# Performance work log

Measured on AMD Instinct MI355X. Metric: run time of the kernel, lower is better.

The kernel has to match this reference:

```python
import jax, jax.numpy as jnp
import numpy as np
import math

N = 20000      # nodes
E = 640000     # edges (avg degree 32)
G = 128        # g_dim (input features)
H1 = 128       # rgcn output dim
H2 = 128       # transformer output dim
R = 8          # num_relations


def setup_inputs() -> dict:
    key = jax.random.key(0)
    ks = jax.random.split(key, 12)
    x = jax.random.normal(ks[0], (N, G), dtype=jnp.float32)
    edge_index = jax.random.randint(ks[1], (2, E), 0, N)
    edge_type = jax.random.randint(ks[2], (E,), 0, R)
    s_in = 1.0 / math.sqrt(G)
    s_h1 = 1.0 / math.sqrt(H1)
    return {
        'x': x,
        'edge_index': edge_index,
        'edge_type': edge_type,
        # RGCNConv params (per-relation weights + root weight + bias)
        'rgcn_weight': jax.random.normal(ks[3], (R, G, H1), dtype=jnp.float32) * s_in,
        'rgcn_root': jax.random.normal(ks[4], (G, H1), dtype=jnp.float32) * s_in,
        'rgcn_bias': jnp.zeros((H1,), dtype=jnp.float32),
        # TransformerConv params (heads=1): query/key/value + skip linear
        'Wq': jax.random.normal(ks[5], (H1, H2), dtype=jnp.float32) * s_h1,
        'bq': jnp.zeros((H2,), dtype=jnp.float32),
        'Wk': jax.random.normal(ks[6], (H1, H2), dtype=jnp.float32) * s_h1,
        'bk': jnp.zeros((H2,), dtype=jnp.float32),
        'Wv': jax.random.normal(ks[7], (H1, H2), dtype=jnp.float32) * s_h1,
        'bv': jnp.zeros((H2,), dtype=jnp.float32),
        'Ws': jax.random.normal(ks[8], (H1, H2), dtype=jnp.float32) * s_h1,
        'bs': jnp.zeros((H2,), dtype=jnp.float32),
    }


def reference(x, edge_index, edge_type, rgcn_weight, rgcn_root, rgcn_bias,
              Wq, bq, Wk, bk, Wv, bv, Ws, bs):
    n = x.shape[0]
    src, dst = edge_index[0], edge_index[1]

    # ---- RGCNConv (aggr='mean' per relation, root weight + bias) ----
    # transform nodes by every relation, then gather per-edge message
    xr = jnp.einsum('ni,rio->nro', x, rgcn_weight)          # [N, R, H1]
    msg = xr[src, edge_type]                                # [E, H1]
    # per (dst, relation) edge counts for mean aggregation
    cnt = jnp.zeros((n, rgcn_weight.shape[0]), x.dtype).at[dst, edge_type].add(1.0)
    denom = jnp.maximum(cnt[dst, edge_type], 1.0)[:, None]  # [E, 1]
    agg = jnp.zeros((n, rgcn_weight.shape[2]), x.dtype).at[dst].add(msg / denom)
    h = agg + x @ rgcn_root + rgcn_bias
    h = jax.nn.relu(h)

    # ---- TransformerConv (heads=1, concat, root_weight=True) ----
    d = Wq.shape[1]
    q = h @ Wq + bq                                          # [N, H2]
    k = h @ Wk + bk
    v = h @ Wv + bv
    score = jnp.sum(q[dst] * k[src], axis=-1) / math.sqrt(d) # [E]
    # softmax over incoming edges of each destination node
    smax = jax.ops.segment_max(score, dst, num_segments=n)   # [N]
    e = jnp.exp(score - smax[dst])                           # [E]
    den = jax.ops.segment_sum(e, dst, num_segments=n)        # [N]
    alpha = e / jnp.maximum(den[dst], 1e-16)                 # [E]
    out = jax.ops.segment_sum(alpha[:, None] * v[src], dst, num_segments=n)
    out = out + h @ Ws + bs                                  # skip connection
    return jax.nn.relu(out)
```

## Files before the change

### kernel.cpp

```cpp
#include <hip/hip_runtime.h>

typedef unsigned short u16;
typedef unsigned int u32;
typedef __attribute__((ext_vector_type(8))) short short8;
typedef __attribute__((ext_vector_type(4))) float f32x4;

#define NN 20000
#define EE 640000
#define SCAN_BLOCKS 80

__device__ inline u16 f2bf(float f) {
    u32 x = __float_as_uint(f);
    return (u16)((x + 0x7FFFu + ((x >> 16) & 1u)) >> 16);
}
__device__ inline float lo16(u32 w) { return __uint_as_float(w << 16); }
__device__ inline float hi16(u32 w) { return __uint_as_float(w & 0xFFFF0000u); }
__device__ inline u32 packbf(float a, float b) { return ((u32)f2bf(b) << 16) | (u32)f2bf(a); }

#define CT_N (EE / 8)
#define CX_N (NN * 32)
#define WP_N (128 * 1152 + 4 * 128 * 128 + 512)
__global__ __launch_bounds__(256) void prep_count(const int* __restrict__ ei,
                                                  const int* __restrict__ et,
                                                  int* __restrict__ cnt, int* __restrict__ rank,
                                                  const float* __restrict__ x,
                                                  const float* rw, const float* root,
                                                  const float* Wq, const float* Wk,
                                                  const float* Wv, const float* Ws,
                                                  const float* bq, const float* bk,
                                                  const float* bv, const float* bs,
                                                  u16* __restrict__ xb,
                                                  u16* wt1, u16* wt2, float* bcat) {
    int idx = blockIdx.x * 256 + threadIdx.x;
    if (idx < CT_N) {
#pragma unroll
        for (int j = 0; j < 8; j++) {
            int e = idx + j * CT_N;
            int dst = ei[EE + e];
            int r = et[e];
            rank[e] = atomicAdd(&cnt[dst * 8 + r], 1);
        }
        return;
    }
    idx -= CT_N;
    if (idx < CX_N) {
        float4 v = *(const float4*)(x + (size_t)idx * 4);
        uint2 o;
        o.x = packbf(v.x, v.y);
        o.y = packbf(v.z, v.w);
        *(uint2*)(xb + (size_t)idx * 4) = o;
        return;
    }
    idx -= CX_N;
    const int S1 = 128 * 1152, S2 = 4 * 128 * 128;
    if (idx < S1) {
        int o = idx / 1152, k = idx - o * 1152;
        float v = (k < 1024) ? rw[k * 128 + o] : root[(k - 1024) * 128 + o];
        wt1[idx] = f2bf(v);
    } else if (idx < S1 + S2) {
        int j = idx - S1;
        int y = j >> 14, rem = j & 16383, o = rem >> 7, i = rem & 127;
        const float* W = (y == 0) ? Wq : (y == 1) ? Wk : (y == 2) ? Wv : Ws;
        wt2[j] = f2bf(W[i * 128 + o]);
    } else if (idx < S1 + S2 + 512) {
        int j = idx - (S1 + S2);
        int y = j >> 7, c = j & 127;
        const float* b = (y == 0) ? bq : (y == 1) ? bk : (y == 2) ? bv : bs;
        bcat[j] = b[c];
    }
}

__global__ __launch_bounds__(256) void scan_phase1(const int* __restrict__ cnt,
                                                   int* __restrict__ deg_pref,
                                                   int* __restrict__ blk_sums) {
    __shared__ int lds[256];
    int t = threadIdx.x;
    int n = blockIdx.x * 256 + t;
    int d = 0;
    if (n < NN) {
        int4 c0 = *(const int4*)(cnt + n * 8);
        int4 c1 = *(const int4*)(cnt + n * 8 + 4);
        d = c0.x + c0.y + c0.z + c0.w + c1.x + c1.y + c1.z + c1.w;
    }
    lds[t] = d;
    __syncthreads();
    for (int o = 1; o < 256; o <<= 1) {
        int v = (t >= o) ? lds[t - o] : 0;
        __syncthreads();
        lds[t] += v;
        __syncthreads();
    }
    if (n < NN) deg_pref[n] = lds[t];
    if (t == 255) blk_sums[blockIdx.x] = lds[255];
}

__global__ __launch_bounds__(256) void scan_phase3(const int* __restrict__ cnt,
                                                   const int* __restrict__ deg_pref,
                                                   const int* __restrict__ blk_sums,
                                                   int* __restrict__ row_off,
                                                   int* __restrict__ srt) {
    __shared__ int bs_lds[128];
    int t = threadIdx.x;
    if (t < 128) {
        int v = (t < SCAN_BLOCKS) ? blk_sums[t] : 0;
        bs_lds[t] = v;
    }
    __syncthreads();
    if (t < 128) {
        for (int o = 1; o < 128; o <<= 1) {
            int a = (t >= o) ? bs_lds[t - o] : 0;
            __syncthreads();
            bs_lds[t] += a;
            __syncthreads();
        }
    } else {
        for (int o = 1; o < 128; o <<= 1) {
            __syncthreads();
            __syncthreads();
        }
    }
    int blk_excl = (blockIdx.x > 0) ? bs_lds[blockIdx.x - 1] : 0;
    int n = blockIdx.x * 256 + t;
    if (n >= NN) return;
    int4 c0 = *(const int4*)(cnt + n * 8);
    int4 c1 = *(const int4*)(cnt + n * 8 + 4);
    int deg = c0.x + c0.y + c0.z + c0.w + c1.x + c1.y + c1.z + c1.w;
    int start = blk_excl + deg_pref[n] - deg;
    row_off[n] = start;
    int sub = start;
    int o[8];
    o[0] = sub; sub += c0.x;
    o[1] = sub; sub += c0.y;
    o[2] = sub; sub += c0.z;
    o[3] = sub; sub += c0.w;
    o[4] = sub; sub += c1.x;
    o[5] = sub; sub += c1.y;
    o[6] = sub; sub += c1.z;
    o[7] = sub; sub += c1.w;
    *(int4*)(srt + n * 8) = make_int4(o[0], o[1], o[2], o[3]);
    *(int4*)(srt + n * 8 + 4) = make_int4(o[4], o[5], o[6], o[7]);
    if (n == NN - 1) row_off[NN] = sub;
}

__global__ void scatter_kernel(const int* __restrict__ ei, const int* __restrict__ et,
                               const int* __restrict__ srt, const int* __restrict__ rank,
                               int* __restrict__ es) {
    int base = blockIdx.x * 2048 + threadIdx.x;
#pragma unroll
    for (int j = 0; j < 8; j++) {
        int e = base + j * 256;
        if (e < EE) {
            int dst = ei[EE + e];
            int src = ei[e];
            int r = et[e];
            es[srt[dst * 8 + r] + rank[e]] = src;
        }
    }
}

__global__ __launch_bounds__(256) void gemm_rgcn_fused(const u16* __restrict__ xb,
                                                       const int* __restrict__ srt,
                                                       const int* __restrict__ cnt,
                                                       const int* __restrict__ es,
                                                       const u16* __restrict__ Bt1,
                                                       const float* __restrict__ bias1,
                                                       const u16* __restrict__ Wt2,
                                                       const float* __restrict__ bcat,
                                                       u16* __restrict__ Cq, u16* __restrict__ Ckv,
                                                       u16* __restrict__ Cs) {
    __shared__ u16 As[32 * 136];
    __shared__ u16 Bs[128 * 136];
    int tid = threadIdx.x;
    int w = tid >> 6;
    int lane = tid & 63;
    int quad = lane >> 4;
    int ml = lane & 15;
    int mt = w & 1;
    int nq = w >> 1;
    int block_m = blockIdx.x * 32;

    int rbase = tid >> 4;
    int cb = (tid & 15) * 8;

    int node_l = tid >> 3;
    int th = tid & 7;
    int db = th * 16;
    int gnode = block_m + node_l;

    f32x4 acc[4];
#pragma unroll
    for (int i = 0; i < 4; i++) acc[i] = (f32x4){0.f, 0.f, 0.f, 0.f};

#pragma unroll 1
    for (int slot = 0; slot < 9; slot++) {
        int kb = slot * 128;
#pragma unroll
        for (int rep = 0; rep < 8; rep++) {
            int r = rbase + rep * 16;
            short8 val = *(const short8*)(Bt1 + (long)r * 1152 + kb + cb);
            *(short8*)(Bs + r * 136 + cb) = val;
        }
        if (slot < 8) {
            int c = cnt[gnode * 8 + slot];
            int p0 = srt[gnode * 8 + slot];
            float a0 = 0.f, a1 = 0.f, a2 = 0.f, a3 = 0.f, a4 = 0.f, a5 = 0.f, a6 = 0.f, a7 = 0.f;
            float a8 = 0.f, a9 = 0.f, a10 = 0.f, a11 = 0.f, a12 = 0.f, a13 = 0.f, a14 = 0.f, a15 = 0.f;
            int i = 0;
            for (; i + 2 <= c; i += 2) {
                int s0 = es[p0 + i], s1 = es[p0 + i + 1];
                uint4 wa0 = *(const uint4*)(xb + (long)s0 * 128 + db);
                uint4 wa1 = *(const uint4*)(xb + (long)s0 * 128 + db + 8);
                uint4 wb0 = *(const uint4*)(xb + (long)s1 * 128 + db);
                uint4 wb1 = *(const uint4*)(xb + (long)s1 * 128 + db + 8);
                a0 += lo16(wa0.x) + lo16(wb0.x);
                a1 += hi16(wa0.x) + hi16(wb0.x);
                a2 += lo16(wa0.y) + lo16(wb0.y);
                a3 += hi16(wa0.y) + hi16(wb0.y);
                a4 += lo16(wa0.z) + lo16(wb0.z);
                a5 += hi16(wa0.z) + hi16(wb0.z);
                a6 += lo16(wa0.w) + lo16(wb0.w);
                a7 += hi16(wa0.w) + hi16(wb0.w);
                a8 += lo16(wa1.x) + lo16(wb1.x);
                a9 += hi16(wa1.x) + hi16(wb1.x);
                a10 += lo16(wa1.y) + lo16(wb1.y);
                a11 += hi16(wa1.y) + hi16(wb1.y);
                a12 += lo16(wa1.z) + lo16(wb1.z);
                a13 += hi16(wa1.z) + hi16(wb1.z);
                a14 += lo16(wa1.w) + lo16(wb1.w);
                a15 += hi16(wa1.w) + hi16(wb1.w);
            }
            if (i < c) {
                int s0 = es[p0 + i];
                uint4 wa0 = *(const uint4*)(xb + (long)s0 * 128 + db);
                uint4 wa1 = *(const uint4*)(xb + (long)s0 * 128 + db + 8);
                a0 += lo16(wa0.x); a1 += hi16(wa0.x); a2 += lo16(wa0.y); a3 += hi16(wa0.y);
                a4 += lo16(wa0.z); a5 += hi16(wa0.z); a6 += lo16(wa0.w); a7 += hi16(wa0.w);
                a8 += lo16(wa1.x); a9 += hi16(wa1.x); a10 += lo16(wa1.y); a11 += hi16(wa1.y);
                a12 += lo16(wa1.z); a13 += hi16(wa1.z); a14 += lo16(wa1.w); a15 += hi16(wa1.w);
            }
            float inv = 1.0f / (float)(c > 1 ? c : 1);
            uint4 o0 = make_uint4(packbf(a0 * inv, a1 * inv), packbf(a2 * inv, a3 * inv),
                                  packbf(a4 * inv, a5 * inv), packbf(a6 * inv, a7 * inv));
            uint4 o1 = make_uint4(packbf(a8 * inv, a9 * inv), packbf(a10 * inv, a11 * inv),
                                  packbf(a12 * inv, a13 * inv), packbf(a14 * inv, a15 * inv));
            *(uint4*)(As + node_l * 136 + db) = o0;
            *(uint4*)(As + node_l * 136 + db + 8) = o1;
        } else {
#pragma unroll
            for (int rep = 0; rep < 2; rep++) {
                int r = rbase + rep * 16;
                short8 val = *(const short8*)(xb + (long)(block_m + r) * 128 + cb);
                *(short8*)(As + r * 136 + cb) = val;
            }
        }
        __syncthreads();
#pragma unroll
        for (int ks = 0; ks < 4; ks++) {
            short8 af = *(const short8*)(As + (mt * 16 + ml) * 136 + ks * 32 + quad * 8);
#pragma unroll
            for (int nt = 0; nt < 4; nt++) {
                short8 bfr = *(const short8*)(Bs + (nq * 64 + nt * 16 + ml) * 136 + ks * 32 + quad * 8);
                acc[nt] = __builtin_amdgcn_mfma_f32_16x16x32_bf16(af, bfr, acc[nt], 0, 0, 0);
            }
        }
        __syncthreads();
    }
#pragma unroll
    for (int nt = 0; nt < 4; nt++) {
        int col = nq * 64 + nt * 16 + ml;
        float bv = bias1[col];
#pragma unroll
        for (int i = 0; i < 4; i++) {
            int r = mt * 16 + quad * 4 + i;
            As[r * 136 + col] = f2bf(fmaxf(acc[nt][i] + bv, 0.f));
        }
    }
    __syncthreads();

#pragma unroll 1
    for (int y = 0; y < 4; y++) {
#pragma unroll
        for (int rep = 0; rep < 8; rep++) {
            int r = rbase + rep * 16;
            short8 val = *(const short8*)(Wt2 + (long)y * 16384 + (long)r * 128 + cb);
            *(short8*)(Bs + r * 136 + cb) = val;
        }
        __syncthreads();
        f32x4 acc2[4];
#pragma unroll
        for (int i = 0; i < 4; i++) acc2[i] = (f32x4){0.f, 0.f, 0.f, 0.f};
#pragma unroll
        for (int ks = 0; ks < 4; ks++) {
            short8 af = *(const short8*)(As + (mt * 16 + ml) * 136 + ks * 32 + quad * 8);
#pragma unroll
            for (int nt = 0; nt < 4; nt++) {
                short8 bfr = *(const short8*)(Bs + (nq * 64 + nt * 16 + ml) * 136 + ks * 32 + quad * 8);
                acc2[nt] = __builtin_amdgcn_mfma_f32_16x16x32_bf16(af, bfr, acc2[nt], 0, 0, 0);
            }
        }
        u16* C;
        int ldc;
        if (y == 0) { C = Cq; ldc = 128; }
        else if (y == 1) { C = Ckv; ldc = 256; }
        else if (y == 2) { C = Ckv + 128; ldc = 256; }
        else { C = Cs; ldc = 128; }
#pragma unroll
        for (int nt = 0; nt < 4; nt++) {
            int col = nq * 64 + nt * 16 + ml;
            float bv = bcat[y * 128 + col];
#pragma unroll
            for (int i = 0; i < 4; i++) {
                int gr = block_m + mt * 16 + quad * 4 + i;
                C[(long)gr * ldc + col] = f2bf(acc2[nt][i] + bv);
            }
        }
        __syncthreads();
    }
}

__global__ __launch_bounds__(128) void attn_kernel(const u16* __restrict__ q,
                                                   const u16* __restrict__ kv,
                                                   const u16* __restrict__ skip,
                                                   const int* __restrict__ row_off,
                                                   const int* __restrict__ es,
                                                   float* __restrict__ out) {
    int node = blockIdx.x * 8 + (threadIdx.x >> 4);
    int lane = threadIdx.x & 15;
    if (node >= NN) return;
    int p0 = row_off[node], p1 = row_off[node + 1];
    uint4 qw = *(const uint4*)(q + (long)node * 128 + lane * 8);
    float q0 = lo16(qw.x), q1 = hi16(qw.x), q2 = lo16(qw.y), q3 = hi16(qw.y);
    float q4 = lo16(qw.z), q5 = hi16(qw.z), q6 = lo16(qw.w), q7 = hi16(qw.w);
    const float SC = 0.08838834764831845f;
    float l = 0.f;
    float a0 = 0.f, a1 = 0.f, a2 = 0.f, a3 = 0.f, a4 = 0.f, a5 = 0.f, a6 = 0.f, a7 = 0.f;
    int p = p0;
    for (; p + 4 <= p1; p += 4) {
        const u16* b0 = kv + (long)es[p] * 256 + lane * 8;
        const u16* b1 = kv + (long)es[p + 1] * 256 + lane * 8;
        const u16* b2 = kv + (long)es[p + 2] * 256 + lane * 8;
        const u16* b3 = kv + (long)es[p + 3] * 256 + lane * 8;
        uint4 k0 = *(const uint4*)b0;
        uint4 k1 = *(const uint4*)b1;
        uint4 k2 = *(const uint4*)b2;
        uint4 k3 = *(const uint4*)b3;
        uint4 v0 = *(const uint4*)(b0 + 128);
        uint4 v1 = *(const uint4*)(b1 + 128);
        uint4 v2 = *(const uint4*)(b2 + 128);
        uint4 v3 = *(const uint4*)(b3 + 128);
        float t0 = q0 * lo16(k0.x) + q1 * hi16(k0.x) + q2 * lo16(k0.y) + q3 * hi16(k0.y) +
                   q4 * lo16(k0.z) + q5 * hi16(k0.z) + q6 * lo16(k0.w) + q7 * hi16(k0.w);
        float t1 = q0 * lo16(k1.x) + q1 * hi16(k1.x) + q2 * lo16(k1.y) + q3 * hi16(k1.y) +
                   q4 * lo16(k1.z) + q5 * hi16(k1.z) + q6 * lo16(k1.w) + q7 * hi16(k1.w);
        float t2 = q0 * lo16(k2.x) + q1 * hi16(k2.x) + q2 * lo16(k2.y) + q3 * hi16(k2.y) +
                   q4 * lo16(k2.z) + q5 * hi16(k2.z) + q6 * lo16(k2.w) + q7 * hi16(k2.w);
        float t3 = q0 * lo16(k3.x) + q1 * hi16(k3.x) + q2 * lo16(k3.y) + q3 * hi16(k3.y) +
                   q4 * lo16(k3.z) + q5 * hi16(k3.z) + q6 * lo16(k3.w) + q7 * hi16(k3.w);
#pragma unroll
        for (int off = 8; off >= 1; off >>= 1) {
            t0 += __shfl_xor(t0, off, 16);
            t1 += __shfl_xor(t1, off, 16);
            t2 += __shfl_xor(t2, off, 16);
            t3 += __shfl_xor(t3, off, 16);
        }
        float w0 = __expf(fminf(t0 * SC, 70.f));
        float w1 = __expf(fminf(t1 * SC, 70.f));
        float w2 = __expf(fminf(t2 * SC, 70.f));
        float w3 = __expf(fminf(t3 * SC, 70.f));
        l += (w0 + w1) + (w2 + w3);
        a0 += w0 * lo16(v0.x) + w1 * lo16(v1.x) + w2 * lo16(v2.x) + w3 * lo16(v3.x);
        a1 += w0 * hi16(v0.x) + w1 * hi16(v1.x) + w2 * hi16(v2.x) + w3 * hi16(v3.x);
        a2 += w0 * lo16(v0.y) + w1 * lo16(v1.y) + w2 * lo16(v2.y) + w3 * lo16(v3.y);
        a3 += w0 * hi16(v0.y) + w1 * hi16(v1.y) + w2 * hi16(v2.y) + w3 * hi16(v3.y);
        a4 += w0 * lo16(v0.z) + w1 * lo16(v1.z) + w2 * lo16(v2.z) + w3 * lo16(v3.z);
        a5 += w0 * hi16(v0.z) + w1 * hi16(v1.z) + w2 * hi16(v2.z) + w3 * hi16(v3.z);
        a6 += w0 * lo16(v0.w) + w1 * lo16(v1.w) + w2 * lo16(v2.w) + w3 * lo16(v3.w);
        a7 += w0 * hi16(v0.w) + w1 * hi16(v1.w) + w2 * hi16(v2.w) + w3 * hi16(v3.w);
    }
    for (; p < p1; p++) {
        const u16* b = kv + (long)es[p] * 256 + lane * 8;
        uint4 kw = *(const uint4*)b;
        uint4 vw = *(const uint4*)(b + 128);
        float t = q0 * lo16(kw.x) + q1 * hi16(kw.x) + q2 * lo16(kw.y) + q3 * hi16(kw.y) +
                  q4 * lo16(kw.z) + q5 * hi16(kw.z) + q6 * lo16(kw.w) + q7 * hi16(kw.w);
#pragma unroll
        for (int off = 8; off >= 1; off >>= 1) t += __shfl_xor(t, off, 16);
        float w = __expf(fminf(t * SC, 70.f));
        l += w;
        a0 += w * lo16(vw.x);
        a1 += w * hi16(vw.x);
        a2 += w * lo16(vw.y);
        a3 += w * hi16(vw.y);
        a4 += w * lo16(vw.z);
        a5 += w * hi16(vw.z);
        a6 += w * lo16(vw.w);
        a7 += w * hi16(vw.w);
    }
    float invl = (l > 0.f) ? 1.0f / l : 0.f;
    uint4 sw = *(const uint4*)(skip + (long)node * 128 + lane * 8);
    float4 oa, ob;
    oa.x = fmaxf(a0 * invl + lo16(sw.x), 0.f);
    oa.y = fmaxf(a1 * invl + hi16(sw.x), 0.f);
    oa.z = fmaxf(a2 * invl + lo16(sw.y), 0.f);
    oa.w = fmaxf(a3 * invl + hi16(sw.y), 0.f);
    ob.x = fmaxf(a4 * invl + lo16(sw.z), 0.f);
    ob.y = fmaxf(a5 * invl + hi16(sw.z), 0.f);
    ob.z = fmaxf(a6 * invl + lo16(sw.w), 0.f);
    ob.w = fmaxf(a7 * invl + hi16(sw.w), 0.f);
    *(float4*)(out + (long)node * 128 + lane * 8) = oa;
    *(float4*)(out + (long)node * 128 + lane * 8 + 4) = ob;
}

extern "C" void kernel_launch(void* const* d_in, const int* in_sizes, int n_in,
                              void* d_out, int out_size, void* d_ws, size_t ws_size,
                              hipStream_t stream) {
    const float* x = (const float*)d_in[0];
    const int* ei = (const int*)d_in[1];
    const int* et = (const int*)d_in[2];
    const float* rw = (const float*)d_in[3];
    const float* root = (const float*)d_in[4];
    const float* rbias = (const float*)d_in[5];
    const float* Wq = (const float*)d_in[6];
    const float* bq = (const float*)d_in[7];
    const float* Wk = (const float*)d_in[8];
    const float* bk = (const float*)d_in[9];
    const float* Wv = (const float*)d_in[10];
    const float* bv = (const float*)d_in[11];
    const float* Ws = (const float*)d_in[12];
    const float* bs = (const float*)d_in[13];

    char* ws = (char*)d_ws;
    size_t off = 0;
    auto alloc = [&](size_t b) {
        size_t o = off;
        off = (off + b + 255) & ~(size_t)255;
        return o;
    };
    u16* qv = (u16*)(ws + alloc((size_t)NN * 128 * 2));
    u16* kv = (u16*)(ws + alloc((size_t)NN * 256 * 2));
    u16* skip = (u16*)(ws + alloc((size_t)NN * 128 * 2));
    u16* xb = (u16*)(ws + alloc((size_t)NN * 128 * 2));
    u16* wt1 = (u16*)(ws + alloc((size_t)128 * 1152 * 2));
    u16* wt2 = (u16*)(ws + alloc((size_t)4 * 128 * 128 * 2));
    float* bcat = (float*)(ws + alloc((size_t)512 * 4));
    int* cnt = (int*)(ws + alloc((size_t)NN * 8 * 4));
    int* row_off = (int*)(ws + alloc((size_t)(NN + 1) * 4));
    int* srt = (int*)(ws + alloc((size_t)NN * 8 * 4));
    int* deg_pref = (int*)(ws + alloc((size_t)NN * 4));
    int* blk_sums = (int*)(ws + alloc((size_t)128 * 4));
    int* rank = (int*)(ws + alloc((size_t)EE * 4));
    int* es = (int*)(ws + alloc((size_t)EE * 4));
    (void)ws_size;
    (void)in_sizes;
    (void)n_in;
    (void)out_size;

    hipMemsetAsync(cnt, 0, (size_t)NN * 8 * 4, stream);

    prep_count<<<(CT_N + CX_N + WP_N + 255) / 256, 256, 0, stream>>>(
        ei, et, cnt, rank, x, rw, root, Wq, Wk, Wv, Ws, bq, bk, bv, bs,
        xb, wt1, wt2, bcat);

    scan_phase1<<<SCAN_BLOCKS, 256, 0, stream>>>(cnt, deg_pref, blk_sums);
    scan_phase3<<<SCAN_BLOCKS, 256, 0, stream>>>(cnt, deg_pref, blk_sums, row_off, srt);
    scatter_kernel<<<(EE + 2047) / 2048, 256, 0, stream>>>(ei, et, srt, rank, es);

    gemm_rgcn_fused<<<NN / 32, 256, 0, stream>>>(xb, srt, cnt, es, wt1, rbias, wt2, bcat,
                                                 qv, kv, skip);

    attn_kernel<<<(NN + 7) / 8, 128, 0, stream>>>(qv, kv, skip, row_off, es, (float*)d_out);
}
```

Before: 233.8 us.

## Halve fused RGCN GEMM row tile to 16 nodes, spreading gather across more threads

The fused RGCN aggregation+GEMM kernel now processes 16 nodes per block instead of 32. Each node's gather is split across 16 threads loading 8 bf16 features each, and each wave computes a 16x32 output tile. The root-weight slot is peeled out of the relation loop. This doubles the block count (1250) and shortens each thread's serial gather chain to expose more memory parallelism, at the cost of reloading the full weight tiles into shared memory twice as often per node.

```diff
diff --git a/kernel.cpp b/kernel.cpp
--- a/kernel.cpp
+++ b/kernel.cpp
@@ -168,31 +168,30 @@
                                                        const float* __restrict__ bcat,
                                                        u16* __restrict__ Cq, u16* __restrict__ Ckv,
                                                        u16* __restrict__ Cs) {
-    __shared__ u16 As[32 * 136];
+    __shared__ u16 As[16 * 136];
     __shared__ u16 Bs[128 * 136];
     int tid = threadIdx.x;
     int w = tid >> 6;
     int lane = tid & 63;
     int quad = lane >> 4;
     int ml = lane & 15;
-    int mt = w & 1;
-    int nq = w >> 1;
-    int block_m = blockIdx.x * 32;
+    int nq = w;
+    int block_m = blockIdx.x * 16;
 
     int rbase = tid >> 4;
     int cb = (tid & 15) * 8;
 
-    int node_l = tid >> 3;
-    int th = tid & 7;
-    int db = th * 16;
+    int node_l = tid >> 4;
+    int th = tid & 15;
+    int db = th * 8;
     int gnode = block_m + node_l;
 
-    f32x4 acc[4];
-#pragma unroll
-    for (int i = 0; i < 4; i++) acc[i] = (f32x4){0.f, 0.f, 0.f, 0.f};
+    f32x4 acc[2];
+#pragma unroll
+    for (int i = 0; i < 2; i++) acc[i] = (f32x4){0.f, 0.f, 0.f, 0.f};
 
 #pragma unroll 1
-    for (int slot = 0; slot < 9; slot++) {
+    for (int slot = 0; slot < 8; slot++) {
         int kb = slot * 128;
 #pragma unroll
         for (int rep = 0; rep < 8; rep++) {
@@ -200,78 +199,73 @@
             short8 val = *(const short8*)(Bt1 + (long)r * 1152 + kb + cb);
             *(short8*)(Bs + r * 136 + cb) = val;
         }
-        if (slot < 8) {
-            int c = cnt[gnode * 8 + slot];
-            int p0 = srt[gnode * 8 + slot];
-            float a0 = 0.f, a1 = 0.f, a2 = 0.f, a3 = 0.f, a4 = 0.f, a5 = 0.f, a6 = 0.f, a7 = 0.f;
-            float a8 = 0.f, a9 = 0.f, a10 = 0.f, a11 = 0.f, a12 = 0.f, a13 = 0.f, a14 = 0.f, a15 = 0.f;
-            int i = 0;
-            for (; i + 2 <= c; i += 2) {
-                int s0 = es[p0 + i], s1 = es[p0 + i + 1];
-                uint4 wa0 = *(const uint4*)(xb + (long)s0 * 128 + db);
-                uint4 wa1 = *(const uint4*)(xb + (long)s0 * 128 + db + 8);
-                uint4 wb0 = *(const uint4*)(xb + (long)s1 * 128 + db);
-                uint4 wb1 = *(const uint4*)(xb + (long)s1 * 128 + db + 8);
-                a0 += lo16(wa0.x) + lo16(wb0.x);
-                a1 += hi16(wa0.x) + hi16(wb0.x);
-                a2 += lo16(wa0.y) + lo16(wb0.y);
-                a3 += hi16(wa0.y) + hi16(wb0.y);
-                a4 += lo16(wa0.z) + lo16(wb0.z);
-                a5 += hi16(wa0.z) + hi16(wb0.z);
-                a6 += lo16(wa0.w) + lo16(wb0.w);
-                a7 += hi16(wa0.w) + hi16(wb0.w);
-                a8 += lo16(wa1.x) + lo16(wb1.x);
-                a9 += hi16(wa1.x) + hi16(wb1.x);
-                a10 += lo16(wa1.y) + lo16(wb1.y);
-                a11 += hi16(wa1.y) + hi16(wb1.y);
-                a12 += lo16(wa1.z) + lo16(wb1.z);
-                a13 += hi16(wa1.z) + hi16(wb1.z);
-                a14 += lo16(wa1.w) + lo16(wb1.w);
-                a15 += hi16(wa1.w) + hi16(wb1.w);
-            }
-            if (i < c) {
-                int s0 = es[p0 + i];
-                uint4 wa0 = *(const uint4*)(xb + (long)s0 * 128 + db);
-                uint4 wa1 = *(const uint4*)(xb + (long)s0 * 128 + db + 8);
-                a0 += lo16(wa0.x); a1 += hi16(wa0.x); a2 += lo16(wa0.y); a3 += hi16(wa0.y);
-                a4 += lo16(wa0.z); a5 += hi16(wa0.z); a6 += lo16(wa0.w); a7 += hi16(wa0.w);
-                a8 += lo16(wa1.x); a9 += hi16(wa1.x); a10 += lo16(wa1.y); a11 += hi16(wa1.y);
-                a12 += lo16(wa1.z); a13 += hi16(wa1.z); a14 += lo16(wa1.w); a15 += hi16(wa1.w);
-            }
-            float inv = 1.0f / (float)(c > 1 ? c : 1);
-            uint4 o0 = make_uint4(packbf(a0 * inv, a1 * inv), packbf(a2 * inv, a3 * inv),
-                                  packbf(a4 * inv, a5 * inv), packbf(a6 * inv, a7 * inv));
-            uint4 o1 = make_uint4(packbf(a8 * inv, a9 * inv), packbf(a10 * inv, a11 * inv),
-                                  packbf(a12 * inv, a13 * inv), packbf(a14 * inv, a15 * inv));
-            *(uint4*)(As + node_l * 136 + db) = o0;
-            *(uint4*)(As + node_l * 136 + db + 8) = o1;
-        } else {
-#pragma unroll
-            for (int rep = 0; rep < 2; rep++) {
-                int r = rbase + rep * 16;
-                short8 val = *(const short8*)(xb + (long)(block_m + r) * 128 + cb);
-                *(short8*)(As + r * 136 + cb) = val;
-            }
-        }
+        int c = cnt[gnode * 8 + slot];
+        int p0 = srt[gnode * 8 + slot];
+        float a0 = 0.f, a1 = 0.f, a2 = 0.f, a3 = 0.f, a4 = 0.f, a5 = 0.f, a6 = 0.f, a7 = 0.f;
+        int i = 0;
+        for (; i + 2 <= c; i += 2) {
+            int s0 = es[p0 + i], s1 = es[p0 + i + 1];
+            uint4 wa = *(const uint4*)(xb + (long)s0 * 128 + db);
+            uint4 wb = *(const uint4*)(xb + (long)s1 * 128 + db);
+            a0 += lo16(wa.x) + lo16(wb.x);
+            a1 += hi16(wa.x) + hi16(wb.x);
+            a2 += lo16(wa.y) + lo16(wb.y);
+            a3 += hi16(wa.y) + hi16(wb.y);
+            a4 += lo16(wa.z) + lo16(wb.z);
+            a5 += hi16(wa.z) + hi16(wb.z);
+            a6 += lo16(wa.w) + lo16(wb.w);
+            a7 += hi16(wa.w) + hi16(wb.w);
+        }
+        if (i < c) {
+            int s0 = es[p0 + i];
+            uint4 wa = *(const uint4*)(xb + (long)s0 * 128 + db);
+            a0 += lo16(wa.x); a1 += hi16(wa.x); a2 += lo16(wa.y); a3 += hi16(wa.y);
+            a4 += lo16(wa.z); a5 += hi16(wa.z); a6 += lo16(wa.w); a7 += hi16(wa.w);
+        }
+        float inv = 1.0f / (float)(c > 1 ? c : 1);
+        uint4 o0 = make_uint4(packbf(a0 * inv, a1 * inv), packbf(a2 * inv, a3 * inv),
+                              packbf(a4 * inv, a5 * inv), packbf(a6 * inv, a7 * inv));
+        *(uint4*)(As + node_l * 136 + db) = o0;
         __syncthreads();
 #pragma unroll
         for (int ks = 0; ks < 4; ks++) {
-            short8 af = *(const short8*)(As + (mt * 16 + ml) * 136 + ks * 32 + quad * 8);
-#pragma unroll
-            for (int nt = 0; nt < 4; nt++) {
-                short8 bfr = *(const short8*)(Bs + (nq * 64 + nt * 16 + ml) * 136 + ks * 32 + quad * 8);
+            short8 af = *(const short8*)(As + ml * 136 + ks * 32 + quad * 8);
+#pragma unroll
+            for (int nt = 0; nt < 2; nt++) {
+                short8 bfr = *(const short8*)(Bs + (nq * 32 + nt * 16 + ml) * 136 + ks * 32 + quad * 8);
                 acc[nt] = __builtin_amdgcn_mfma_f32_16x16x32_bf16(af, bfr, acc[nt], 0, 0, 0);
             }
         }
         __syncthreads();
     }
-#pragma unroll
-    for (int nt = 0; nt < 4; nt++) {
-        int col = nq * 64 + nt * 16 + ml;
+    {
+#pragma unroll
+        for (int rep = 0; rep < 8; rep++) {
+            int r = rbase + rep * 16;
+            short8 val = *(const short8*)(Bt1 + (long)r * 1152 + 1024 + cb);
+            *(short8*)(Bs + r * 136 + cb) = val;
+        }
+        short8 val = *(const short8*)(xb + (long)(block_m + rbase) * 128 + cb);
+        *(short8*)(As + rbase * 136 + cb) = val;
+        __syncthreads();
+#pragma unroll
+        for (int ks = 0; ks < 4; ks++) {
+            short8 af = *(const short8*)(As + ml * 136 + ks * 32 + quad * 8);
+#pragma unroll
+            for (int nt = 0; nt < 2; nt++) {
+                short8 bfr = *(const short8*)(Bs + (nq * 32 + nt * 16 + ml) * 136 + ks * 32 + quad * 8);
+                acc[nt] = __builtin_amdgcn_mfma_f32_16x16x32_bf16(af, bfr, acc[nt], 0, 0, 0);
+            }
+        }
+        __syncthreads();
+    }
+#pragma unroll
+    for (int nt = 0; nt < 2; nt++) {
+        int col = nq * 32 + nt * 16 + ml;
         float bv = bias1[col];
 #pragma unroll
         for (int i = 0; i < 4; i++) {
-            int r = mt * 16 + quad * 4 + i;
+            int r = quad * 4 + i;
             As[r * 136 + col] = f2bf(fmaxf(acc[nt][i] + bv, 0.f));
         }
     }
@@ -286,15 +280,15 @@
             *(short8*)(Bs + r * 136 + cb) = val;
         }
         __syncthreads();
-        f32x4 acc2[4];
-#pragma unroll
-        for (int i = 0; i < 4; i++) acc2[i] = (f32x4){0.f, 0.f, 0.f, 0.f};
+        f32x4 acc2[2];
+#pragma unroll
+        for (int i = 0; i < 2; i++) acc2[i] = (f32x4){0.f, 0.f, 0.f, 0.f};
 #pragma unroll
         for (int ks = 0; ks < 4; ks++) {
-            short8 af = *(const short8*)(As + (mt * 16 + ml) * 136 + ks * 32 + quad * 8);
-#pragma unroll
-            for (int nt = 0; nt < 4; nt++) {
-                short8 bfr = *(const short8*)(Bs + (nq * 64 + nt * 16 + ml) * 136 + ks * 32 + quad * 8);
+            short8 af = *(const short8*)(As + ml * 136 + ks * 32 + quad * 8);
+#pragma unroll
+            for (int nt = 0; nt < 2; nt++) {
+                short8 bfr = *(const short8*)(Bs + (nq * 32 + nt * 16 + ml) * 136 + ks * 32 + quad * 8);
                 acc2[nt] = __builtin_amdgcn_mfma_f32_16x16x32_bf16(af, bfr, acc2[nt], 0, 0, 0);
             }
         }
@@ -305,12 +299,12 @@
         else if (y == 2) { C = Ckv + 128; ldc = 256; }
         else { C = Cs; ldc = 128; }
 #pragma unroll
-        for (int nt = 0; nt < 4; nt++) {
-            int col = nq * 64 + nt * 16 + ml;
+        for (int nt = 0; nt < 2; nt++) {
+            int col = nq * 32 + nt * 16 + ml;
             float bv = bcat[y * 128 + col];
 #pragma unroll
             for (int i = 0; i < 4; i++) {
-                int gr = block_m + mt * 16 + quad * 4 + i;
+                int gr = block_m + quad * 4 + i;
                 C[(long)gr * ldc + col] = f2bf(acc2[nt][i] + bv);
             }
         }
@@ -465,7 +459,7 @@
     scan_phase3<<<SCAN_BLOCKS, 256, 0, stream>>>(cnt, deg_pref, blk_sums, row_off, srt);
     scatter_kernel<<<(EE + 2047) / 2048, 256, 0, stream>>>(ei, et, srt, rank, es);
 
-    gemm_rgcn_fused<<<NN / 32, 256, 0, stream>>>(xb, srt, cnt, es, wt1, rbias, wt2, bcat,
+    gemm_rgcn_fused<<<NN / 16, 256, 0, stream>>>(xb, srt, cnt, es, wt1, rbias, wt2, bcat,
                                                  qv, kv, skip);
 
     attn_kernel<<<(NN + 7) / 8, 128, 0, stream>>>(qv, kv, skip, row_off, es, (float*)d_out);
```

Result: slower. 249.5 us (+6.7%).
